# Optimization experiments

Measured on AMD Instinct MI355X. Metric: run time of the kernel, lower is better.

## Reference

```python
import jax, jax.numpy as jnp
import numpy as np

N = 100000
E = 3200000
NFEAT = 512
NHID = 256


def setup_inputs() -> dict:
    key = jax.random.key(0)
    ks = jax.random.split(key, 8)
    x = jax.random.normal(ks[0], (N, NFEAT), dtype=jnp.float32)
    edge_row = jax.random.randint(ks[1], (E,), 0, N, dtype=jnp.int32)
    edge_col = jax.random.randint(ks[2], (E,), 0, N, dtype=jnp.int32)
    edge_val = jax.random.uniform(ks[3], (E,), dtype=jnp.float32)
    # xavier_uniform init as in reset_parameters
    lim1 = np.sqrt(6.0 / (NFEAT + NHID)).astype(np.float32)
    lim2 = np.sqrt(6.0 / (NHID + NHID)).astype(np.float32)
    W1 = jax.random.uniform(ks[4], (NFEAT, NHID), minval=-lim1, maxval=lim1, dtype=jnp.float32)
    W2 = jax.random.uniform(ks[5], (NHID, NHID), minval=-lim2, maxval=lim2, dtype=jnp.float32)
    b1 = jnp.zeros((NHID,), dtype=jnp.float32)
    b2 = jnp.zeros((NHID,), dtype=jnp.float32)
    alpha = jnp.full((1,), 0.25, dtype=jnp.float32)  # PReLU single weight
    return {"x": x, "edge_row": edge_row, "edge_col": edge_col,
            "edge_val": edge_val, "W1": W1, "b1": b1, "W2": W2, "b2": b2,
            "alpha": alpha}


def _spmm(edge_row, edge_col, edge_val, support):
    # out[i] = sum over edges e with row[e]==i of val[e] * support[col[e]]
    msgs = support[edge_col] * edge_val[:, None]  # [E, F]
    return jax.ops.segment_sum(msgs, edge_row, num_segments=N)


def _prelu(x, alpha):
    return jnp.where(x >= 0, x, alpha * x)


def reference(x, edge_row, edge_col, edge_val, W1, b1, W2, b2, alpha):
    # Layer 1: GraphConvolution(nfeat, nhid) -> PReLU (dropout=0 -> identity)
    h = _spmm(edge_row, edge_col, edge_val, x @ W1) + b1
    h = _prelu(h, alpha)
    # Layer 2: GraphConvolution(nhid, nhid) -> PReLU
    h = _spmm(edge_row, edge_col, edge_val, h @ W2) + b2
    h = _prelu(h, alpha)
    return h
```

## Files before the change

### kernel.cpp

```cpp
#include <hip/hip_runtime.h>

#define NHID 256

typedef __attribute__((ext_vector_type(8))) short short8;
typedef __attribute__((ext_vector_type(4))) float floatx4;
typedef __attribute__((ext_vector_type(4))) float float4v;
typedef __attribute__((ext_vector_type(4))) int int4v;
typedef __attribute__((ext_vector_type(4))) unsigned int uint4v;

static __device__ __forceinline__ short f2bf(float f) {
    unsigned u = __float_as_uint(f);
    unsigned r = (u + 0x7fffu + ((u >> 16) & 1u)) >> 16;
    return (short)r;
}
static __device__ __forceinline__ unsigned pk2(float a, float b) {
    return ((unsigned)(unsigned short)f2bf(a)) | (((unsigned)(unsigned short)f2bf(b)) << 16);
}

__global__ void transpose_cast(const float* __restrict__ W, short* __restrict__ Wt, int K)
{
    int idx = blockIdx.x * 256 + threadIdx.x;
    if (idx >= K * NHID) return;
    int k = idx >> 8;
    int n = idx & 255;
    Wt[(size_t)n * K + k] = f2bf(W[idx]);
}

template<bool ABF16>
__global__ __launch_bounds__(512) void gemm_mfma(
    const void* __restrict__ Ap, const short* __restrict__ Bt,
    short* __restrict__ C, int M, int K)
{
    __shared__ __align__(16) short As[128][40];
    __shared__ __align__(16) short Bs[256][40];

    int tid  = threadIdx.x;
    int m0   = blockIdx.x * 128;
    int lane = tid & 63;
    int wid  = tid >> 6;
    int wm   = wid >> 2;
    int wn   = wid & 3;
    int quad = lane >> 4;
    int l16  = lane & 15;

    floatx4 acc[4][4] = {};

    for (int k0 = 0; k0 < K; k0 += 32) {
        if (ABF16) {
            const short* A = (const short*)Ap;
            int tr = tid >> 2, tc = (tid & 3) * 8;
            int gm = m0 + tr;
            int4v v = {0, 0, 0, 0};
            if (gm < M) v = __builtin_nontemporal_load((const int4v*)(A + (size_t)gm * K + k0 + tc));
            *(int4v*)&As[tr][tc] = v;
        } else {
            const float* A = (const float*)Ap;
            int tr = tid >> 3, tc = (tid & 7) * 4;
            #pragma unroll
            for (int p = 0; p < 2; ++p) {
                int m = p * 64 + tr, gm = m0 + m;
                float4v v = {0.f, 0.f, 0.f, 0.f};
                if (gm < M) v = __builtin_nontemporal_load((const float4v*)(A + (size_t)gm * K + k0 + tc));
                short4 s;
                s.x = f2bf(v.x); s.y = f2bf(v.y); s.z = f2bf(v.z); s.w = f2bf(v.w);
                *(short4*)&As[m][tc] = s;
            }
        }
        {
            int nr = tid >> 2, nc = (tid & 3) * 8;
            #pragma unroll
            for (int p = 0; p < 2; ++p) {
                int n = p * 128 + nr;
                *(int4*)&Bs[n][nc] = *(const int4*)(Bt + (size_t)n * K + k0 + nc);
            }
        }
        __syncthreads();

        short8 af[4], bfr[4];
        #pragma unroll
        for (int t = 0; t < 4; ++t) {
            af[t]  = *(const short8*)&As[wm * 64 + t * 16 + l16][quad * 8];
            bfr[t] = *(const short8*)&Bs[wn * 64 + t * 16 + l16][quad * 8];
        }
        #pragma unroll
        for (int tm = 0; tm < 4; ++tm)
            #pragma unroll
            for (int tn = 0; tn < 4; ++tn)
                acc[tm][tn] = __builtin_amdgcn_mfma_f32_16x16x32_bf16(
                    af[tm], bfr[tn], acc[tm][tn], 0, 0, 0);
        __syncthreads();
    }

    #pragma unroll
    for (int tm = 0; tm < 4; ++tm) {
        #pragma unroll
        for (int r = 0; r < 4; ++r) {
            int row = m0 + wm * 64 + tm * 16 + quad * 4 + r;
            if (row < M) {
                #pragma unroll
                for (int tn = 0; tn < 4; ++tn) {
                    int col = wn * 64 + tn * 16 + l16;
                    C[(size_t)row * NHID + col] = f2bf(acc[tm][tn][r]);
                }
            }
        }
    }
}

__global__ void hist_kernel(const int* __restrict__ rows, int* __restrict__ counts, int E)
{
    int i = blockIdx.x * blockDim.x + threadIdx.x;
    if (i < E) atomicAdd(&counts[rows[i]], 1);
}

__global__ __launch_bounds__(256) void block_scan(
    const int* __restrict__ counts, int* __restrict__ tmp, int* __restrict__ bsum, int n)
{
    __shared__ int ws[4];
    int tid = threadIdx.x, b = blockIdx.x;
    int i = b * 256 + tid;
    int lane = tid & 63, w = tid >> 6;
    int v = (i < n) ? counts[i] : 0;
    int x = v;
    #pragma unroll
    for (int off = 1; off < 64; off <<= 1) {
        int y = __shfl_up(x, off, 64);
        if (lane >= off) x += y;
    }
    if (lane == 63) ws[w] = x;
    __syncthreads();
    int add = 0;
    #pragma unroll
    for (int k = 0; k < 4; ++k) if (k < w) add += ws[k];
    x += add;
    if (i < n) tmp[i] = x;
    if (tid == 255) bsum[b] = x;
}

__global__ __launch_bounds__(256) void scan_bsums(int* __restrict__ bsum, int nb)
{
    __shared__ int ws[4];
    __shared__ int carry;
    int tid = threadIdx.x, lane = tid & 63, w = tid >> 6;
    if (tid == 0) carry = 0;
    __syncthreads();
    for (int base = 0; base < nb; base += 256) {
        int i = base + tid;
        int v = (i < nb) ? bsum[i] : 0;
        int x = v;
        #pragma unroll
        for (int off = 1; off < 64; off <<= 1) {
            int y = __shfl_up(x, off, 64);
            if (lane >= off) x += y;
        }
        if (lane == 63) ws[w] = x;
        __syncthreads();
        int add = 0;
        #pragma unroll
        for (int k = 0; k < 4; ++k) if (k < w) add += ws[k];
        int incl = x + add;
        int c = carry;
        if (i < nb) bsum[i] = incl - v + c;
        __syncthreads();
        if (tid == 255) carry = c + incl;
        __syncthreads();
    }
}

__global__ void finalize_scan(const int* __restrict__ tmp, const int* __restrict__ boff,
                              int* __restrict__ row_ptr, int n)
{
    int i = blockIdx.x * 256 + threadIdx.x;
    if (i < n) row_ptr[i + 1] = tmp[i] + boff[i >> 8];
    if (i == 0) row_ptr[0] = 0;
}

__global__ void scatter_kernel(
    const int* __restrict__ erow, const int* __restrict__ ecol,
    const float* __restrict__ eval, const int* __restrict__ row_ptr,
    int* __restrict__ fill, int2* __restrict__ ep, int E)
{
    int i = blockIdx.x * blockDim.x + threadIdx.x;
    if (i < E) {
        int r = erow[i];
        int p = row_ptr[r] + atomicAdd(&fill[r], 1);
        ep[p] = make_int2(ecol[i], __float_as_int(eval[i]));
    }
}

static __device__ __forceinline__ void fma8(float* acc, uint4 g, float v)
{
    acc[0] += v * __uint_as_float(g.x << 16);
    acc[1] += v * __uint_as_float(g.x & 0xffff0000u);
    acc[2] += v * __uint_as_float(g.y << 16);
    acc[3] += v * __uint_as_float(g.y & 0xffff0000u);
    acc[4] += v * __uint_as_float(g.z << 16);
    acc[5] += v * __uint_as_float(g.z & 0xffff0000u);
    acc[6] += v * __uint_as_float(g.w << 16);
    acc[7] += v * __uint_as_float(g.w & 0xffff0000u);
}

static __device__ __forceinline__ int2 ld_ep(const int2* p)
{
    long long t = __builtin_nontemporal_load((const long long*)p);
    int2 r;
    r.x = (int)(t & 0xffffffffLL);
    r.y = (int)(t >> 32);
    return r;
}

template<bool OUT_BF16>
__global__ __launch_bounds__(256) void spmm_split(
    const int* __restrict__ row_ptr, const int2* __restrict__ ep,
    const short* __restrict__ dense,
    const float* __restrict__ bias, const float* __restrict__ alpha_p,
    void* __restrict__ outp, int nrows)
{
    int wid  = (blockIdx.x * blockDim.x + threadIdx.x) >> 6;
    int lane = threadIdx.x & 63;
    if (wid >= nrows) return;
    int half = lane >> 5;
    int l32  = lane & 31;
    int s = row_ptr[wid], e = row_ptr[wid + 1];
    int fo = l32 * 8;

    float acc[8] = {};
    int i = s;
    for (; i + 7 < e; i += 8) {
        int2 e0 = ld_ep(&ep[i + half]);
        int2 e1 = ld_ep(&ep[i + 2 + half]);
        int2 e2 = ld_ep(&ep[i + 4 + half]);
        int2 e3 = ld_ep(&ep[i + 6 + half]);
        uint4 g0 = *(const uint4*)(dense + (size_t)e0.x * NHID + fo);
        uint4 g1 = *(const uint4*)(dense + (size_t)e1.x * NHID + fo);
        uint4 g2 = *(const uint4*)(dense + (size_t)e2.x * NHID + fo);
        uint4 g3 = *(const uint4*)(dense + (size_t)e3.x * NHID + fo);
        fma8(acc, g0, __int_as_float(e0.y));
        fma8(acc, g1, __int_as_float(e1.y));
        fma8(acc, g2, __int_as_float(e2.y));
        fma8(acc, g3, __int_as_float(e3.y));
    }
    for (; i + 3 < e; i += 4) {
        int2 e0 = ld_ep(&ep[i + half]);
        int2 e1 = ld_ep(&ep[i + 2 + half]);
        uint4 g0 = *(const uint4*)(dense + (size_t)e0.x * NHID + fo);
        uint4 g1 = *(const uint4*)(dense + (size_t)e1.x * NHID + fo);
        fma8(acc, g0, __int_as_float(e0.y));
        fma8(acc, g1, __int_as_float(e1.y));
    }
    for (; i < e; i += 2) {
        int j = i + half;
        if (j < e) {
            int2 e0 = ld_ep(&ep[j]);
            uint4 g0 = *(const uint4*)(dense + (size_t)e0.x * NHID + fo);
            fma8(acc, g0, __int_as_float(e0.y));
        }
    }

    #pragma unroll
    for (int k = 0; k < 8; ++k) acc[k] += __shfl_xor(acc[k], 32, 64);

    float alpha = alpha_p[0];
    float4 b0 = *(const float4*)(bias + fo);
    float4 b1 = *(const float4*)(bias + fo + 4);
    float r[8];
    r[0] = acc[0] + b0.x; r[1] = acc[1] + b0.y; r[2] = acc[2] + b0.z; r[3] = acc[3] + b0.w;
    r[4] = acc[4] + b1.x; r[5] = acc[5] + b1.y; r[6] = acc[6] + b1.z; r[7] = acc[7] + b1.w;
    #pragma unroll
    for (int k = 0; k < 8; ++k) r[k] = (r[k] >= 0.f) ? r[k] : alpha * r[k];

    if (OUT_BF16) {
        if (half == 0) {
            uint4v o;
            o.x = pk2(r[0], r[1]); o.y = pk2(r[2], r[3]);
            o.z = pk2(r[4], r[5]); o.w = pk2(r[6], r[7]);
            __builtin_nontemporal_store(o, (uint4v*)((short*)outp + (size_t)wid * NHID + fo));
        }
    } else {
        float4v ov;
        if (half) { ov.x = r[4]; ov.y = r[5]; ov.z = r[6]; ov.w = r[7]; }
        else      { ov.x = r[0]; ov.y = r[1]; ov.z = r[2]; ov.w = r[3]; }
        __builtin_nontemporal_store(ov, (float4v*)((float*)outp + (size_t)wid * NHID + fo + half * 4));
    }
}

extern "C" void kernel_launch(void* const* d_in, const int* in_sizes, int n_in,
                              void* d_out, int out_size, void* d_ws, size_t ws_size,
                              hipStream_t stream)
{
    const float* x     = (const float*)d_in[0];
    const int*   erow  = (const int*)d_in[1];
    const int*   ecol  = (const int*)d_in[2];
    const float* eval  = (const float*)d_in[3];
    const float* W1    = (const float*)d_in[4];
    const float* b1    = (const float*)d_in[5];
    const float* W2    = (const float*)d_in[6];
    const float* b2    = (const float*)d_in[7];
    const float* alpha = (const float*)d_in[8];

    int NFEAT = 512;
    int N = in_sizes[0] / NFEAT;
    int E = in_sizes[1];
    float* out = (float*)d_out;

    char* wsp = (char*)d_ws;
    short* support_b = (short*)wsp;  wsp += (size_t)N * NHID * sizeof(short);
    short* h1b       = (short*)wsp;  wsp += (size_t)N * NHID * sizeof(short);
    int2*  ep        = (int2*)wsp;   wsp += (size_t)E * sizeof(int2);
    int*   row_ptr   = (int*)wsp;    wsp += ((size_t)(N + 1) * sizeof(int) + 15) & ~(size_t)15;
    short* W1t       = (short*)wsp;  wsp += (size_t)NFEAT * NHID * sizeof(short);
    short* W2t       = (short*)wsp;  wsp += (size_t)NHID * NHID * sizeof(short);

    int* fill = (int*)h1b;
    int* tmp  = fill + N;
    int* bsum = tmp + N;
    int  nblk = (N + 255) / 256;

    transpose_cast<<<(NFEAT * NHID + 255) / 256, 256, 0, stream>>>(W1, W1t, NFEAT);
    transpose_cast<<<(NHID * NHID + 255) / 256, 256, 0, stream>>>(W2, W2t, NHID);

    hipMemsetAsync(fill, 0, (size_t)N * sizeof(int), stream);
    hist_kernel<<<(E + 255) / 256, 256, 0, stream>>>(erow, fill, E);
    block_scan<<<nblk, 256, 0, stream>>>(fill, tmp, bsum, N);
    scan_bsums<<<1, 256, 0, stream>>>(bsum, nblk);
    finalize_scan<<<nblk, 256, 0, stream>>>(tmp, bsum, row_ptr, N);
    hipMemsetAsync(fill, 0, (size_t)N * sizeof(int), stream);
    scatter_kernel<<<(E + 255) / 256, 256, 0, stream>>>(erow, ecol, eval, row_ptr, fill, ep, E);

    int  ggrid = (N + 127) / 128;
    int  spmm_blocks = (N + 3) / 4;

    gemm_mfma<false><<<ggrid, 512, 0, stream>>>(x, W1t, support_b, N, NFEAT);
    spmm_split<true><<<spmm_blocks, 256, 0, stream>>>(row_ptr, ep, support_b, b1, alpha, h1b, N);
    gemm_mfma<true><<<ggrid, 512, 0, stream>>>(h1b, W2t, support_b, N, NHID);
    spmm_split<false><<<spmm_blocks, 256, 0, stream>>>(row_ptr, ep, support_b, b2, alpha, out, N);
}
```

Measured before the change: 1.146 ms.

## Merge weight casts, fill CSR via atomicSub, and launch SpMM one row per block

Merges the two weight transpose-cast kernels into a single launch. The CSR scatter now decrements a per-row end pointer, which removes one memset and the row_ptr read. The SpMM kernels launch one 64-thread block per row instead of four rows per 256-thread block, drop the 8-edge unrolled loop, and use plain loads instead of nontemporal loads for edge pairs. Fewer launches and less setup work are traded against less memory-level parallelism in SpMM and more blocks to schedule.

New measurement: 1.212 ms. +5.8%, slower.

```diff
diff --git a/kernel.cpp b/kernel.cpp
--- a/kernel.cpp
+++ b/kernel.cpp
@@ -17,13 +17,24 @@
     return ((unsigned)(unsigned short)f2bf(a)) | (((unsigned)(unsigned short)f2bf(b)) << 16);
 }
 
-__global__ void transpose_cast(const float* __restrict__ W, short* __restrict__ Wt, int K)
+__global__ void transpose_cast2(const float* __restrict__ W1, short* __restrict__ W1t,
+                                const float* __restrict__ W2, short* __restrict__ W2t,
+                                int K1, int K2)
 {
     int idx = blockIdx.x * 256 + threadIdx.x;
-    if (idx >= K * NHID) return;
-    int k = idx >> 8;
-    int n = idx & 255;
-    Wt[(size_t)n * K + k] = f2bf(W[idx]);
+    int n1 = K1 * NHID;
+    if (idx < n1) {
+        int k = idx >> 8;
+        int n = idx & 255;
+        W1t[(size_t)n * K1 + k] = f2bf(W1[idx]);
+    } else {
+        int j = idx - n1;
+        if (j < K2 * NHID) {
+            int k = j >> 8;
+            int n = j & 255;
+            W2t[(size_t)n * K2 + k] = f2bf(W2[j]);
+        }
+    }
 }
 
 template<bool ABF16>
@@ -168,22 +179,26 @@
 }
 
 __global__ void finalize_scan(const int* __restrict__ tmp, const int* __restrict__ boff,
-                              int* __restrict__ row_ptr, int n)
+                              int* __restrict__ row_ptr, int* __restrict__ rowend, int n)
 {
     int i = blockIdx.x * 256 + threadIdx.x;
-    if (i < n) row_ptr[i + 1] = tmp[i] + boff[i >> 8];
+    if (i < n) {
+        int v = tmp[i] + boff[i >> 8];
+        row_ptr[i + 1] = v;
+        rowend[i] = v;
+    }
     if (i == 0) row_ptr[0] = 0;
 }
 
 __global__ void scatter_kernel(
     const int* __restrict__ erow, const int* __restrict__ ecol,
-    const float* __restrict__ eval, const int* __restrict__ row_ptr,
-    int* __restrict__ fill, int2* __restrict__ ep, int E)
+    const float* __restrict__ eval,
+    int* __restrict__ rowend, int2* __restrict__ ep, int E)
 {
     int i = blockIdx.x * blockDim.x + threadIdx.x;
     if (i < E) {
         int r = erow[i];
-        int p = row_ptr[r] + atomicAdd(&fill[r], 1);
+        int p = atomicSub(&rowend[r], 1) - 1;
         ep[p] = make_int2(ecol[i], __float_as_int(eval[i]));
     }
 }
@@ -200,24 +215,15 @@
     acc[7] += v * __uint_as_float(g.w & 0xffff0000u);
 }
 
-static __device__ __forceinline__ int2 ld_ep(const int2* p)
-{
-    long long t = __builtin_nontemporal_load((const long long*)p);
-    int2 r;
-    r.x = (int)(t & 0xffffffffLL);
-    r.y = (int)(t >> 32);
-    return r;
-}
-
 template<bool OUT_BF16>
-__global__ __launch_bounds__(256) void spmm_split(
+__global__ __launch_bounds__(64) void spmm_split(
     const int* __restrict__ row_ptr, const int2* __restrict__ ep,
     const short* __restrict__ dense,
     const float* __restrict__ bias, const float* __restrict__ alpha_p,
     void* __restrict__ outp, int nrows)
 {
-    int wid  = (blockIdx.x * blockDim.x + threadIdx.x) >> 6;
-    int lane = threadIdx.x & 63;
+    int wid  = blockIdx.x;
+    int lane = threadIdx.x;
     if (wid >= nrows) return;
     int half = lane >> 5;
     int l32  = lane & 31;
@@ -226,23 +232,9 @@
 
     float acc[8] = {};
     int i = s;
-    for (; i + 7 < e; i += 8) {
-        int2 e0 = ld_ep(&ep[i + half]);
-        int2 e1 = ld_ep(&ep[i + 2 + half]);
-        int2 e2 = ld_ep(&ep[i + 4 + half]);
-        int2 e3 = ld_ep(&ep[i + 6 + half]);
-        uint4 g0 = *(const uint4*)(dense + (size_t)e0.x * NHID + fo);
-        uint4 g1 = *(const uint4*)(dense + (size_t)e1.x * NHID + fo);
-        uint4 g2 = *(const uint4*)(dense + (size_t)e2.x * NHID + fo);
-        uint4 g3 = *(const uint4*)(dense + (size_t)e3.x * NHID + fo);
-        fma8(acc, g0, __int_as_float(e0.y));
-        fma8(acc, g1, __int_as_float(e1.y));
-        fma8(acc, g2, __int_as_float(e2.y));
-        fma8(acc, g3, __int_as_float(e3.y));
-    }
     for (; i + 3 < e; i += 4) {
-        int2 e0 = ld_ep(&ep[i + half]);
-        int2 e1 = ld_ep(&ep[i + 2 + half]);
+        int2 e0 = ep[i + half];
+        int2 e1 = ep[i + 2 + half];
         uint4 g0 = *(const uint4*)(dense + (size_t)e0.x * NHID + fo);
         uint4 g1 = *(const uint4*)(dense + (size_t)e1.x * NHID + fo);
         fma8(acc, g0, __int_as_float(e0.y));
@@ -251,7 +243,7 @@
     for (; i < e; i += 2) {
         int j = i + half;
         if (j < e) {
-            int2 e0 = ld_ep(&ep[j]);
+            int2 e0 = ep[j];
             uint4 g0 = *(const uint4*)(dense + (size_t)e0.x * NHID + fo);
             fma8(acc, g0, __int_as_float(e0.y));
         }
@@ -311,27 +303,26 @@
     short* W1t       = (short*)wsp;  wsp += (size_t)NFEAT * NHID * sizeof(short);
     short* W2t       = (short*)wsp;  wsp += (size_t)NHID * NHID * sizeof(short);
 
-    int* fill = (int*)h1b;
-    int* tmp  = fill + N;
-    int* bsum = tmp + N;
+    int* counts = (int*)h1b;
+    int* tmp    = counts + N;
+    int* bsum   = tmp + N;
+    int* rowend = bsum + ((N + 255) / 256);
     int  nblk = (N + 255) / 256;
 
-    transpose_cast<<<(NFEAT * NHID + 255) / 256, 256, 0, stream>>>(W1, W1t, NFEAT);
-    transpose_cast<<<(NHID * NHID + 255) / 256, 256, 0, stream>>>(W2, W2t, NHID);
-
-    hipMemsetAsync(fill, 0, (size_t)N * sizeof(int), stream);
-    hist_kernel<<<(E + 255) / 256, 256, 0, stream>>>(erow, fill, E);
-    block_scan<<<nblk, 256, 0, stream>>>(fill, tmp, bsum, N);
+    transpose_cast2<<<((NFEAT + NHID) * NHID + 255) / 256, 256, 0, stream>>>(
+        W1, W1t, W2, W2t, NFEAT, NHID);
+
+    hipMemsetAsync(counts, 0, (size_t)N * sizeof(int), stream);
+    hist_kernel<<<(E + 255) / 256, 256, 0, stream>>>(erow, counts, E);
+    block_scan<<<nblk, 256, 0, stream>>>(counts, tmp, bsum, N);
     scan_bsums<<<1, 256, 0, stream>>>(bsum, nblk);
-    finalize_scan<<<nblk, 256, 0, stream>>>(tmp, bsum, row_ptr, N);
-    hipMemsetAsync(fill, 0, (size_t)N * sizeof(int), stream);
-    scatter_kernel<<<(E + 255) / 256, 256, 0, stream>>>(erow, ecol, eval, row_ptr, fill, ep, E);
+    finalize_scan<<<nblk, 256, 0, stream>>>(tmp, bsum, row_ptr, rowend, N);
+    scatter_kernel<<<(E + 255) / 256, 256, 0, stream>>>(erow, ecol, eval, rowend, ep, E);
 
     int  ggrid = (N + 127) / 128;
-    int  spmm_blocks = (N + 3) / 4;
 
     gemm_mfma<false><<<ggrid, 512, 0, stream>>>(x, W1t, support_b, N, NFEAT);
-    spmm_split<true><<<spmm_blocks, 256, 0, stream>>>(row_ptr, ep, support_b, b1, alpha, h1b, N);
+    spmm_split<true><<<N, 64, 0, stream>>>(row_ptr, ep, support_b, b1, alpha, h1b, N);
     gemm_mfma<true><<<ggrid, 512, 0, stream>>>(h1b, W2t, support_b, N, NHID);
-    spmm_split<false><<<spmm_blocks, 256, 0, stream>>>(row_ptr, ep, support_b, b2, alpha, out, N);
-}
+    spmm_split<false><<<N, 64, 0, stream>>>(row_ptr, ep, support_b, b2, alpha, out, N);
+}
```
